# Optimization experiments

Hardware: AMD Instinct MI355X
Metric: run time of the kernel (lower is better)

The kernel has to match this reference:

```python
import jax, jax.numpy as jnp
import numpy as np

B, T, D, H = 4, 2048, 1024, 16
HD = D // H


def setup_inputs() -> dict:
    key = jax.random.key(0)
    ks = jax.random.split(key, 6)
    s = 0.02
    return {
        "x": jax.random.normal(ks[0], (B, T, D), dtype=jnp.float32),
        "padding_mask": jnp.zeros((B, T), dtype=bool),
        "Wq": jax.random.normal(ks[1], (D, D), dtype=jnp.float32) * s,
        "Wk": jax.random.normal(ks[2], (D, D), dtype=jnp.float32) * s,
        "Wv": jax.random.normal(ks[3], (D, D), dtype=jnp.float32) * s,
        "Wo": jax.random.normal(ks[4], (D, D), dtype=jnp.float32) * s,
        "bo": jax.random.normal(ks[5], (D,), dtype=jnp.float32) * s,
    }


def reference(x, padding_mask, Wq, Wk, Wv, Wo, bo):
    # torch nn.Linear: y = x @ W.T
    b, t, d = x.shape
    q = (x @ Wq.T).reshape(b, t, H, HD).transpose(0, 2, 1, 3)  # [B,H,T,hd]
    k = (x @ Wk.T).reshape(b, t, H, HD).transpose(0, 2, 1, 3)
    v = (x @ Wv.T).reshape(b, t, H, HD).transpose(0, 2, 1, 3)

    scores = jnp.einsum("bhid,bhjd->bhij", q, k) / jnp.sqrt(jnp.float32(HD))
    causal = jnp.tril(jnp.ones((t, t), dtype=bool))  # [T,T]
    neg_inf = jnp.float32(-jnp.inf)
    scores = jnp.where(causal[None, None, :, :], scores, neg_inf)
    scores = jnp.where(padding_mask[:, None, None, :], neg_inf, scores)

    attn = jax.nn.softmax(scores, axis=-1)
    out = jnp.einsum("bhij,bhjd->bhid", attn, v)
    out = out.transpose(0, 2, 1, 3).reshape(b, t, d)
    out = out @ Wo.T + bo
    nonpad = (~padding_mask)[:, :, None].astype(out.dtype)
    return out * nonpad
```

## Files before the change

kernel.cpp:

```cpp
#include <hip/hip_runtime.h>

#define B_ 4
#define T_ 2048
#define D_ 1024
#define H_ 16
#define BT_ (B_ * T_)
#define QSCALE (0.125f * 1.44269504088896f)

typedef unsigned short u16;
typedef __attribute__((ext_vector_type(8))) __bf16 bf16x8;
typedef __attribute__((ext_vector_type(4))) float f32x4;

__device__ __forceinline__ u16 f2bf(float f) {
  unsigned u = __builtin_bit_cast(unsigned, f);
  u += 0x7FFFu + ((u >> 16) & 1u);
  return (u16)(u >> 16);
}

__device__ __forceinline__ void gload16(const void* g, void* l) {
  __builtin_amdgcn_global_load_lds(
      (const __attribute__((address_space(1))) void*)g,
      (__attribute__((address_space(3))) void*)l, 16, 0, 0);
}

__global__ void cvt_bf16(const float* __restrict__ in, u16* __restrict__ out, int n4) {
  int i = blockIdx.x * 256 + threadIdx.x;
  if (i >= n4) return;
  const float4 v = ((const float4*)in)[i];
  ushort4 o;
  o.x = f2bf(v.x); o.y = f2bf(v.y); o.z = f2bf(v.z); o.w = f2bf(v.w);
  ((ushort4*)out)[i] = o;
}

__global__ void cvt_wts(const float* __restrict__ Wq, const float* __restrict__ Wk,
                        const float* __restrict__ Wv, const float* __restrict__ Wo,
                        u16* __restrict__ wdst,
                        const unsigned char* __restrict__ pm, unsigned char* __restrict__ fl) {
  const int by = blockIdx.y;
  if (by < 4) {
    const float* src = (by == 0) ? Wq : (by == 1) ? Wk : (by == 2) ? Wv : Wo;
    const int i = blockIdx.x * 256 + threadIdx.x;
    const float4 v = ((const float4*)src)[i];
    ushort4 o;
    o.x = f2bf(v.x); o.y = f2bf(v.y); o.z = f2bf(v.z); o.w = f2bf(v.w);
    ((ushort4*)(wdst + (size_t)by * D_ * D_))[i] = o;
  } else if (blockIdx.x == 0 && threadIdx.x < 128) {
    const int i = threadIdx.x;
    const unsigned long long* p = (const unsigned long long*)(pm + i * 64);
    unsigned long long acc = 0;
#pragma unroll
    for (int k = 0; k < 8; ++k) acc |= p[k];
    fl[i] = acc ? 1 : 0;
  }
}

template<int MODE>
__global__ __launch_bounds__(256, 2) void gemm_bt(
    const u16* __restrict__ A, const u16* __restrict__ Bw,
    float* __restrict__ Cf, const float* __restrict__ bias,
    const unsigned char* __restrict__ rowmask,
    u16* __restrict__ Cq, u16* __restrict__ Ck, u16* __restrict__ Cvt)
{
  __shared__ __align__(16) u16 sA[128 * 64];
  __shared__ __align__(16) u16 sB[128 * 64];
  const int tid = threadIdx.x;
  const int lane = tid & 63, wave = tid >> 6;
  const int g = lane >> 4, s15 = lane & 15;
  const int bm = blockIdx.x * 128, bn = blockIdx.y * 128;
  const int wr = wave >> 1, wc = wave & 1;

  const int srow = lane >> 3;
  const int scol = ((lane & 7) ^ srow) << 3;

  f32x4 acc[4][4] = {};

  for (int kt = 0; kt < 16; ++kt) {
    __syncthreads();
    const int k0 = kt << 6;
#pragma unroll
    for (int c = 0; c < 4; ++c) {
      const int chunk = c * 4 + wave;
      gload16(A  + (size_t)(bm + chunk * 8 + srow) * 1024 + k0 + scol, (char*)sA + chunk * 1024);
      gload16(Bw + (size_t)(bn + chunk * 8 + srow) * 1024 + k0 + scol, (char*)sB + chunk * 1024);
    }
    __syncthreads();
#pragma unroll
    for (int kk = 0; kk < 2; ++kk) {
      const int cb = ((kk << 6) | (g << 4)) ^ ((s15 & 7) << 4);
      bf16x8 af[4], bf[4];
#pragma unroll
      for (int mm = 0; mm < 4; ++mm)
        af[mm] = *(const bf16x8*)((const char*)sA + (wr * 64 + mm * 16 + s15) * 128 + cb);
#pragma unroll
      for (int nn = 0; nn < 4; ++nn)
        bf[nn] = *(const bf16x8*)((const char*)sB + (wc * 64 + nn * 16 + s15) * 128 + cb);
#pragma unroll
      for (int mm = 0; mm < 4; ++mm)
#pragma unroll
        for (int nn = 0; nn < 4; ++nn)
          acc[mm][nn] = __builtin_amdgcn_mfma_f32_16x16x32_bf16(af[mm], bf[nn], acc[mm][nn], 0, 0, 0);
    }
  }

  if (MODE == 1) {
    const int region = bn >> 10;
    const float a = (region == 0) ? QSCALE : 1.f;
#pragma unroll
    for (int mm = 0; mm < 4; ++mm)
#pragma unroll
      for (int nn = 0; nn < 4; ++nn) {
        const int col = bn + wc * 64 + nn * 16 + s15;
        const int colr = col & 1023;
        const int row0 = bm + wr * 64 + mm * 16 + (g << 2);
        if (region == 2) {
          ushort4 w;
          w.x = f2bf(acc[mm][nn][0]); w.y = f2bf(acc[mm][nn][1]);
          w.z = f2bf(acc[mm][nn][2]); w.w = f2bf(acc[mm][nn][3]);
          *(ushort4*)(Cvt + (size_t)colr * BT_ + row0) = w;
        } else {
          u16* dst = region ? Ck : Cq;
#pragma unroll
          for (int r = 0; r < 4; ++r)
            dst[(size_t)(row0 + r) * 1024 + colr] = f2bf(acc[mm][nn][r] * a);
        }
      }
  } else {
#pragma unroll
    for (int mm = 0; mm < 4; ++mm)
#pragma unroll
      for (int nn = 0; nn < 4; ++nn) {
        const int col = bn + wc * 64 + nn * 16 + s15;
        const int row0 = bm + wr * 64 + mm * 16 + (g << 2);
        const float bv = bias[col];
#pragma unroll
        for (int r = 0; r < 4; ++r) {
          float v = acc[mm][nn][r] + bv;
          v = rowmask[row0 + r] ? 0.f : v;
          Cf[(size_t)(row0 + r) * 1024 + col] = v;
        }
      }
  }
}

__global__ __launch_bounds__(512, 4) void attn_fwd(
    const u16* __restrict__ Q, const u16* __restrict__ K,
    const u16* __restrict__ VT, const unsigned char* __restrict__ pm,
    const unsigned char* __restrict__ tileflag, u16* __restrict__ O)
{
  __shared__ __align__(16) u16 sK[2][64 * 64];
  __shared__ __align__(16) u16 sV[2][64 * 64];
  const int tid = threadIdx.x;
  const int lane = tid & 63, wave = tid >> 6;
  const int g = lane >> 4, s15 = lane & 15;
  const int bh = blockIdx.x, b = bh >> 4, h = bh & 15;
  const int qt = blockIdx.y;
  const size_t tokbase = (size_t)b * T_;

  const int srow = tid >> 3;
  const int sc = (tid & 7) ^ (srow & 7);
  const u16* Kb0 = K + tokbase * D_ + h * 64 + sc * 8;
  const u16* Vb0 = VT + (size_t)(h * 64) * BT_ + tokbase + sc * 8;

  const int q0 = qt * 128;
  const int qw = q0 + wave * 16;
  const int nt = 2 * qt + 2;

  bf16x8 qf[2];
#pragma unroll
  for (int ks = 0; ks < 2; ++ks)
    qf[ks] = *(const bf16x8*)(Q + (tokbase + qw + s15) * D_ + h * 64 + ks * 32 + g * 8);

  f32x4 o[4] = {};
  float l_ = 0.f;

  gload16(Kb0 + (size_t)srow * D_,  (char*)(&sK[0][0]) + tid * 16);
  gload16(Vb0 + (size_t)srow * BT_, (char*)(&sV[0][0]) + tid * 16);
  __syncthreads();

  for (int t = 0; t < nt; ++t) {
    const int kv0 = t << 6;
    if (t + 1 < nt) {
      const int nb = (t + 1) & 1;
      gload16(Kb0 + (size_t)(kv0 + 64 + srow) * D_,  (char*)(&sK[nb][0]) + tid * 16);
      gload16(Vb0 + (size_t)srow * BT_ + kv0 + 64,   (char*)(&sV[nb][0]) + tid * 16);
    }

    if (kv0 <= qw + 15) {
      const u16* kb_ = &sK[t & 1][0];
      const u16* vb_ = &sV[t & 1][0];

      f32x4 st[4] = {};
#pragma unroll
      for (int ks = 0; ks < 2; ++ks) {
        bf16x8 kf[4];
#pragma unroll
        for (int jf = 0; jf < 4; ++jf)
          kf[jf] = *(const bf16x8*)(kb_ + (jf * 16 + s15) * 64 + (((ks * 4 + g) ^ (s15 & 7)) << 3));
        __builtin_amdgcn_s_setprio(1);
#pragma unroll
        for (int jf = 0; jf < 4; ++jf)
          st[jf] = __builtin_amdgcn_mfma_f32_16x16x32_bf16(kf[jf], qf[ks], st[jf], 0, 0, 0);
        __builtin_amdgcn_s_setprio(0);
      }

      if (kv0 + 63 > qw) {
        const int iq = qw + s15;
#pragma unroll
        for (int jf = 0; jf < 4; ++jf) {
          const int jb = kv0 + jf * 16 + g * 4;
#pragma unroll
          for (int r = 0; r < 4; ++r)
            if (jb + r > iq) st[jf][r] = -1e30f;
        }
      }
      if (tileflag[b * 32 + t]) {
#pragma unroll
        for (int jf = 0; jf < 4; ++jf) {
          const int jb = kv0 + jf * 16 + g * 4;
          uchar4 p4 = *(const uchar4*)(pm + b * T_ + jb);
          const unsigned char* pr = (const unsigned char*)&p4;
#pragma unroll
          for (int r = 0; r < 4; ++r)
            if (pr[r]) st[jf][r] = -1e30f;
        }
      }

#pragma unroll
      for (int jf = 0; jf < 4; ++jf)
#pragma unroll
        for (int r = 0; r < 4; ++r) {
          const float p = __builtin_amdgcn_exp2f(st[jf][r]);
          st[jf][r] = p;
          l_ += p;
        }

#pragma unroll
      for (int kb2 = 0; kb2 < 2; ++kb2) {
        bf16x8 vf[4];
#pragma unroll
        for (int df = 0; df < 4; ++df)
          vf[df] = *(const bf16x8*)(vb_ + (df * 16 + s15) * 64 + (((kb2 * 4 + g) ^ (s15 & 7)) << 3));
        unsigned w00, w01, w10, w11;
        asm("v_cvt_pk_bf16_f32 %0, %1, %2" : "=v"(w00) : "v"(st[2*kb2][0]),   "v"(st[2*kb2][1]));
        asm("v_cvt_pk_bf16_f32 %0, %1, %2" : "=v"(w01) : "v"(st[2*kb2][2]),   "v"(st[2*kb2][3]));
        asm("v_cvt_pk_bf16_f32 %0, %1, %2" : "=v"(w10) : "v"(st[2*kb2+1][0]), "v"(st[2*kb2+1][1]));
        asm("v_cvt_pk_bf16_f32 %0, %1, %2" : "=v"(w11) : "v"(st[2*kb2+1][2]), "v"(st[2*kb2+1][3]));
        asm("v_permlane32_swap_b32 %0, %1" : "+v"(w00), "+v"(w10));
        asm("v_permlane16_swap_b32 %0, %1" : "+v"(w00), "+v"(w10));
        asm("v_permlane32_swap_b32 %0, %1" : "+v"(w01), "+v"(w11));
        asm("v_permlane16_swap_b32 %0, %1" : "+v"(w01), "+v"(w11));
        union { unsigned u[4]; bf16x8 v; } pf;
        pf.u[0] = w00; pf.u[1] = w01; pf.u[2] = w10; pf.u[3] = w11;
        __builtin_amdgcn_s_setprio(1);
#pragma unroll
        for (int df = 0; df < 4; ++df)
          o[df] = __builtin_amdgcn_mfma_f32_16x16x32_bf16(vf[df], pf.v, o[df], 0, 0, 0);
        __builtin_amdgcn_s_setprio(0);
      }
    }
    __syncthreads();
  }

  l_ += __shfl_xor(l_, 16);
  l_ += __shfl_xor(l_, 32);
  const float inv = 1.f / l_;
  u16* orow = O + (tokbase + qw + s15) * D_ + h * 64 + g * 4;
#pragma unroll
  for (int df = 0; df < 4; ++df) {
    ushort4 w;
    w.x = f2bf(o[df][0] * inv); w.y = f2bf(o[df][1] * inv);
    w.z = f2bf(o[df][2] * inv); w.w = f2bf(o[df][3] * inv);
    *(ushort4*)(orow + df * 16) = w;
  }
}

extern "C" void kernel_launch(void* const* d_in, const int* in_sizes, int n_in,
                              void* d_out, int out_size, void* d_ws, size_t ws_size,
                              hipStream_t stream)
{
  const float* x  = (const float*)d_in[0];
  const unsigned char* pm = (const unsigned char*)d_in[1];
  const float* Wq = (const float*)d_in[2];
  const float* Wk = (const float*)d_in[3];
  const float* Wv = (const float*)d_in[4];
  const float* Wo = (const float*)d_in[5];
  const float* bo = (const float*)d_in[6];
  float* out = (float*)d_out;

  char* w = (char*)d_ws;
  u16* xb  = (u16*)w; w += (size_t)BT_ * D_ * 2;
  u16* wqb = (u16*)w; w += (size_t)D_ * D_ * 2;
  u16* wkb = (u16*)w; w += (size_t)D_ * D_ * 2;
  u16* wvb = (u16*)w; w += (size_t)D_ * D_ * 2;
  u16* wob = (u16*)w; w += (size_t)D_ * D_ * 2;
  u16* qb  = (u16*)w; w += (size_t)BT_ * D_ * 2;
  u16* kbf = (u16*)w; w += (size_t)BT_ * D_ * 2;
  u16* vt  = (u16*)w; w += (size_t)BT_ * D_ * 2;
  u16* ao  = (u16*)w; w += (size_t)BT_ * D_ * 2;
  unsigned char* flags = (unsigned char*)w; w += 256;
  (void)wkb; (void)wvb;

  const int nx4 = BT_ * D_ / 4;
  cvt_bf16<<<nx4 / 256, 256, 0, stream>>>(x, xb, nx4);
  cvt_wts<<<dim3(1024, 5), 256, 0, stream>>>(Wq, Wk, Wv, Wo, wqb, pm, flags);

  gemm_bt<1><<<dim3(64, 24), 256, 0, stream>>>(xb, wqb, nullptr, nullptr, nullptr, qb, kbf, vt);

  attn_fwd<<<dim3(B_ * H_, 16), 512, 0, stream>>>(qb, kbf, vt, pm, flags, ao);

  gemm_bt<0><<<dim3(64, 8), 256, 0, stream>>>(ao, wob, out, bo, pm, nullptr, nullptr, nullptr);
}
```

Baseline: 149.9 us.

## Pair causal query tiles per block and software-pipeline QK with 4-stage KV ring

Each attention block now processes two query tiles (qt and 15-qt) so causal work is balanced across blocks, halving the grid. The KV staging grows from double to quad buffering with loads issued three tiles ahead and explicit vmcnt waits instead of full syncthreads. The QK MFMA for the next tile is computed before the softmax/PV of the current tile to overlap matrix and vector work, and padding tile flags are preloaded into registers. This raises LDS use and register pressure, which may reduce occupancy.

```diff
diff --git a/kernel.cpp b/kernel.cpp
--- a/kernel.cpp
+++ b/kernel.cpp
@@ -8,6 +8,7 @@
 #define QSCALE (0.125f * 1.44269504088896f)
 
 typedef unsigned short u16;
+typedef unsigned long long u64;
 typedef __attribute__((ext_vector_type(8))) __bf16 bf16x8;
 typedef __attribute__((ext_vector_type(4))) float f32x4;
 
@@ -142,18 +143,113 @@
   }
 }
 
+#define QK_TILE(T, ST) do {                                                    \
+  const int kvq_ = (T) << 6;                                                   \
+  _Pragma("unroll")                                                            \
+  for (int jf_ = 0; jf_ < 4; ++jf_) ST[jf_] = f32x4{};                         \
+  if (kvq_ <= qw + 15) {                                                       \
+    const u16* kbq_ = &sK[(T) & 3][0];                                         \
+    _Pragma("unroll")                                                          \
+    for (int ks_ = 0; ks_ < 2; ++ks_) {                                        \
+      bf16x8 kf_[4];                                                           \
+      _Pragma("unroll")                                                        \
+      for (int jf_ = 0; jf_ < 4; ++jf_)                                        \
+        kf_[jf_] = *(const bf16x8*)(kbq_ + (jf_ * 16 + s15) * 64 +             \
+                                    (((ks_ * 4 + g) ^ (s15 & 7)) << 3));       \
+      __builtin_amdgcn_s_setprio(1);                                           \
+      _Pragma("unroll")                                                        \
+      for (int jf_ = 0; jf_ < 4; ++jf_)                                        \
+        ST[jf_] = __builtin_amdgcn_mfma_f32_16x16x32_bf16(kf_[jf_], qf[ks_],   \
+                                                          ST[jf_], 0, 0, 0);   \
+      __builtin_amdgcn_s_setprio(0);                                           \
+    }                                                                          \
+  }                                                                            \
+} while (0)
+
+#define ATTN_ITER(T, CUR, NXT) do {                                            \
+  const int kv0_ = (T) << 6;                                                   \
+  if ((T) + 3 < nt) {                                                          \
+    const int s_ = ((T) + 3) & 3;                                              \
+    gload16(Kb0 + (size_t)(kv0_ + 192 + srow) * D_, (char*)(&sK[s_][0]) + tid * 16); \
+    gload16(Vb0 + (size_t)srow * BT_ + kv0_ + 192,  (char*)(&sV[s_][0]) + tid * 16); \
+  }                                                                            \
+  if ((T) + 1 < nt) QK_TILE((T) + 1, NXT);                                     \
+  if (kv0_ <= qw + 15) {                                                       \
+    if (kv0_ + 63 > qw) {                                                      \
+      const int iq_ = qw + s15;                                                \
+      _Pragma("unroll")                                                        \
+      for (int jf_ = 0; jf_ < 4; ++jf_) {                                      \
+        const int jb_ = kv0_ + jf_ * 16 + g * 4;                               \
+        _Pragma("unroll")                                                      \
+        for (int r_ = 0; r_ < 4; ++r_)                                         \
+          if (jb_ + r_ > iq_) CUR[jf_][r_] = -1e30f;                           \
+      }                                                                        \
+    }                                                                          \
+    if ((flq[(T) >> 3] >> (((T) & 7) * 8)) & 0xff) {                           \
+      _Pragma("unroll")                                                        \
+      for (int jf_ = 0; jf_ < 4; ++jf_) {                                      \
+        const int jb_ = kv0_ + jf_ * 16 + g * 4;                               \
+        uchar4 p4_ = *(const uchar4*)(pm + b * T_ + jb_);                      \
+        const unsigned char* pr_ = (const unsigned char*)&p4_;                 \
+        _Pragma("unroll")                                                      \
+        for (int r_ = 0; r_ < 4; ++r_)                                         \
+          if (pr_[r_]) CUR[jf_][r_] = -1e30f;                                  \
+      }                                                                        \
+    }                                                                          \
+    _Pragma("unroll")                                                          \
+    for (int jf_ = 0; jf_ < 4; ++jf_) {                                        \
+      _Pragma("unroll")                                                        \
+      for (int r_ = 0; r_ < 4; ++r_)                                           \
+        CUR[jf_][r_] = __builtin_amdgcn_exp2f(CUR[jf_][r_]);                   \
+      l4 += CUR[jf_];                                                          \
+    }                                                                          \
+    const u16* vbq_ = &sV[(T) & 3][0];                                         \
+    _Pragma("unroll")                                                          \
+    for (int kb_ = 0; kb_ < 2; ++kb_) {                                        \
+      bf16x8 vf_[4];                                                           \
+      _Pragma("unroll")                                                        \
+      for (int df_ = 0; df_ < 4; ++df_)                                        \
+        vf_[df_] = *(const bf16x8*)(vbq_ + (df_ * 16 + s15) * 64 +             \
+                                    (((kb_ * 4 + g) ^ (s15 & 7)) << 3));       \
+      unsigned w00, w01, w10, w11;                                             \
+      asm("v_cvt_pk_bf16_f32 %0, %1, %2" : "=v"(w00) : "v"(CUR[2*kb_][0]),   "v"(CUR[2*kb_][1]));   \
+      asm("v_cvt_pk_bf16_f32 %0, %1, %2" : "=v"(w01) : "v"(CUR[2*kb_][2]),   "v"(CUR[2*kb_][3]));   \
+      asm("v_cvt_pk_bf16_f32 %0, %1, %2" : "=v"(w10) : "v"(CUR[2*kb_+1][0]), "v"(CUR[2*kb_+1][1])); \
+      asm("v_cvt_pk_bf16_f32 %0, %1, %2" : "=v"(w11) : "v"(CUR[2*kb_+1][2]), "v"(CUR[2*kb_+1][3])); \
+      asm("v_permlane32_swap_b32 %0, %1" : "+v"(w00), "+v"(w10));              \
+      asm("v_permlane16_swap_b32 %0, %1" : "+v"(w00), "+v"(w10));              \
+      asm("v_permlane32_swap_b32 %0, %1" : "+v"(w01), "+v"(w11));              \
+      asm("v_permlane16_swap_b32 %0, %1" : "+v"(w01), "+v"(w11));              \
+      union { unsigned u[4]; bf16x8 v; } pf_;                                  \
+      pf_.u[0] = w00; pf_.u[1] = w01; pf_.u[2] = w10; pf_.u[3] = w11;          \
+      __builtin_amdgcn_s_setprio(1);                                           \
+      _Pragma("unroll")                                                        \
+      for (int df_ = 0; df_ < 4; ++df_)                                        \
+        o[df_] = __builtin_amdgcn_mfma_f32_16x16x32_bf16(vf_[df_], pf_.v,      \
+                                                         o[df_], 0, 0, 0);     \
+      __builtin_amdgcn_s_setprio(0);                                           \
+    }                                                                          \
+  }                                                                            \
+  if ((T) + 1 < nt) {                                                          \
+    if ((T) + 3 < nt) asm volatile("s_waitcnt vmcnt(2) lgkmcnt(0)" ::: "memory"); \
+    else              asm volatile("s_waitcnt vmcnt(0) lgkmcnt(0)" ::: "memory"); \
+    __builtin_amdgcn_s_barrier();                                              \
+    asm volatile("" ::: "memory");                                             \
+  }                                                                            \
+} while (0)
+
 __global__ __launch_bounds__(512, 4) void attn_fwd(
     const u16* __restrict__ Q, const u16* __restrict__ K,
     const u16* __restrict__ VT, const unsigned char* __restrict__ pm,
     const unsigned char* __restrict__ tileflag, u16* __restrict__ O)
 {
-  __shared__ __align__(16) u16 sK[2][64 * 64];
-  __shared__ __align__(16) u16 sV[2][64 * 64];
+  __shared__ __align__(16) u16 sK[4][64 * 64];
+  __shared__ __align__(16) u16 sV[4][64 * 64];
   const int tid = threadIdx.x;
   const int lane = tid & 63, wave = tid >> 6;
   const int g = lane >> 4, s15 = lane & 15;
   const int bh = blockIdx.x, b = bh >> 4, h = bh & 15;
-  const int qt = blockIdx.y;
+  const int jpair = blockIdx.y;
   const size_t tokbase = (size_t)b * T_;
 
   const int srow = tid >> 3;
@@ -161,116 +257,54 @@
   const u16* Kb0 = K + tokbase * D_ + h * 64 + sc * 8;
   const u16* Vb0 = VT + (size_t)(h * 64) * BT_ + tokbase + sc * 8;
 
-  const int q0 = qt * 128;
-  const int qw = q0 + wave * 16;
-  const int nt = 2 * qt + 2;
-
-  bf16x8 qf[2];
-#pragma unroll
-  for (int ks = 0; ks < 2; ++ks)
-    qf[ks] = *(const bf16x8*)(Q + (tokbase + qw + s15) * D_ + h * 64 + ks * 32 + g * 8);
-
-  f32x4 o[4] = {};
-  float l_ = 0.f;
-
-  gload16(Kb0 + (size_t)srow * D_,  (char*)(&sK[0][0]) + tid * 16);
-  gload16(Vb0 + (size_t)srow * BT_, (char*)(&sV[0][0]) + tid * 16);
-  __syncthreads();
-
-  for (int t = 0; t < nt; ++t) {
-    const int kv0 = t << 6;
-    if (t + 1 < nt) {
-      const int nb = (t + 1) & 1;
-      gload16(Kb0 + (size_t)(kv0 + 64 + srow) * D_,  (char*)(&sK[nb][0]) + tid * 16);
-      gload16(Vb0 + (size_t)srow * BT_ + kv0 + 64,   (char*)(&sV[nb][0]) + tid * 16);
-    }
-
-    if (kv0 <= qw + 15) {
-      const u16* kb_ = &sK[t & 1][0];
-      const u16* vb_ = &sV[t & 1][0];
-
-      f32x4 st[4] = {};
-#pragma unroll
-      for (int ks = 0; ks < 2; ++ks) {
-        bf16x8 kf[4];
-#pragma unroll
-        for (int jf = 0; jf < 4; ++jf)
-          kf[jf] = *(const bf16x8*)(kb_ + (jf * 16 + s15) * 64 + (((ks * 4 + g) ^ (s15 & 7)) << 3));
-        __builtin_amdgcn_s_setprio(1);
-#pragma unroll
-        for (int jf = 0; jf < 4; ++jf)
-          st[jf] = __builtin_amdgcn_mfma_f32_16x16x32_bf16(kf[jf], qf[ks], st[jf], 0, 0, 0);
-        __builtin_amdgcn_s_setprio(0);
-      }
-
-      if (kv0 + 63 > qw) {
-        const int iq = qw + s15;
-#pragma unroll
-        for (int jf = 0; jf < 4; ++jf) {
-          const int jb = kv0 + jf * 16 + g * 4;
-#pragma unroll
-          for (int r = 0; r < 4; ++r)
-            if (jb + r > iq) st[jf][r] = -1e30f;
-        }
-      }
-      if (tileflag[b * 32 + t]) {
-#pragma unroll
-        for (int jf = 0; jf < 4; ++jf) {
-          const int jb = kv0 + jf * 16 + g * 4;
-          uchar4 p4 = *(const uchar4*)(pm + b * T_ + jb);
-          const unsigned char* pr = (const unsigned char*)&p4;
-#pragma unroll
-          for (int r = 0; r < 4; ++r)
-            if (pr[r]) st[jf][r] = -1e30f;
-        }
-      }
-
-#pragma unroll
-      for (int jf = 0; jf < 4; ++jf)
-#pragma unroll
-        for (int r = 0; r < 4; ++r) {
-          const float p = __builtin_amdgcn_exp2f(st[jf][r]);
-          st[jf][r] = p;
-          l_ += p;
-        }
-
-#pragma unroll
-      for (int kb2 = 0; kb2 < 2; ++kb2) {
-        bf16x8 vf[4];
-#pragma unroll
-        for (int df = 0; df < 4; ++df)
-          vf[df] = *(const bf16x8*)(vb_ + (df * 16 + s15) * 64 + (((kb2 * 4 + g) ^ (s15 & 7)) << 3));
-        unsigned w00, w01, w10, w11;
-        asm("v_cvt_pk_bf16_f32 %0, %1, %2" : "=v"(w00) : "v"(st[2*kb2][0]),   "v"(st[2*kb2][1]));
-        asm("v_cvt_pk_bf16_f32 %0, %1, %2" : "=v"(w01) : "v"(st[2*kb2][2]),   "v"(st[2*kb2][3]));
-        asm("v_cvt_pk_bf16_f32 %0, %1, %2" : "=v"(w10) : "v"(st[2*kb2+1][0]), "v"(st[2*kb2+1][1]));
-        asm("v_cvt_pk_bf16_f32 %0, %1, %2" : "=v"(w11) : "v"(st[2*kb2+1][2]), "v"(st[2*kb2+1][3]));
-        asm("v_permlane32_swap_b32 %0, %1" : "+v"(w00), "+v"(w10));
-        asm("v_permlane16_swap_b32 %0, %1" : "+v"(w00), "+v"(w10));
-        asm("v_permlane32_swap_b32 %0, %1" : "+v"(w01), "+v"(w11));
-        asm("v_permlane16_swap_b32 %0, %1" : "+v"(w01), "+v"(w11));
-        union { unsigned u[4]; bf16x8 v; } pf;
-        pf.u[0] = w00; pf.u[1] = w01; pf.u[2] = w10; pf.u[3] = w11;
-        __builtin_amdgcn_s_setprio(1);
-#pragma unroll
-        for (int df = 0; df < 4; ++df)
-          o[df] = __builtin_amdgcn_mfma_f32_16x16x32_bf16(vf[df], pf.v, o[df], 0, 0, 0);
-        __builtin_amdgcn_s_setprio(0);
-      }
-    }
+  u64 flq[4];
+#pragma unroll
+  for (int q = 0; q < 4; ++q) flq[q] = ((const u64*)(tileflag + b * 32))[q];
+
+#pragma unroll
+  for (int half = 0; half < 2; ++half) {
+    const int qt = half ? (15 - jpair) : jpair;
+    const int qw = qt * 128 + wave * 16;
+    const int nt = 2 * qt + 2;
+
+    bf16x8 qf[2];
+#pragma unroll
+    for (int ks = 0; ks < 2; ++ks)
+      qf[ks] = *(const bf16x8*)(Q + (tokbase + qw + s15) * D_ + h * 64 + ks * 32 + g * 8);
+
+    f32x4 o[4] = {};
+    f32x4 l4 = {};
+
     __syncthreads();
-  }
-
-  l_ += __shfl_xor(l_, 16);
-  l_ += __shfl_xor(l_, 32);
-  const float inv = 1.f / l_;
-  u16* orow = O + (tokbase + qw + s15) * D_ + h * 64 + g * 4;
-#pragma unroll
-  for (int df = 0; df < 4; ++df) {
-    ushort4 w;
-    w.x = f2bf(o[df][0] * inv); w.y = f2bf(o[df][1] * inv);
-    w.z = f2bf(o[df][2] * inv); w.w = f2bf(o[df][3] * inv);
-    *(ushort4*)(orow + df * 16) = w;
+#pragma unroll
+    for (int s = 0; s < 3; ++s) {
+      gload16(Kb0 + (size_t)(s * 64 + srow) * D_, (char*)(&sK[s][0]) + tid * 16);
+      gload16(Vb0 + (size_t)srow * BT_ + s * 64,  (char*)(&sV[s][0]) + tid * 16);
+    }
+    asm volatile("s_waitcnt vmcnt(2) lgkmcnt(0)" ::: "memory");
+    __builtin_amdgcn_s_barrier();
+    asm volatile("" ::: "memory");
+
+    f32x4 stA[4], stB[4];
+    QK_TILE(0, stA);
+
+    for (int t = 0; t < nt; t += 2) {
+      ATTN_ITER(t, stA, stB);
+      ATTN_ITER(t + 1, stB, stA);
+    }
+
+    float lv = (l4[0] + l4[1]) + (l4[2] + l4[3]);
+    lv += __shfl_xor(lv, 16);
+    lv += __shfl_xor(lv, 32);
+    const float inv = 1.f / lv;
+    u16* orow = O + (tokbase + qw + s15) * D_ + h * 64 + g * 4;
+#pragma unroll
+    for (int df = 0; df < 4; ++df) {
+      ushort4 w;
+      w.x = f2bf(o[df][0] * inv); w.y = f2bf(o[df][1] * inv);
+      w.z = f2bf(o[df][2] * inv); w.w = f2bf(o[df][3] * inv);
+      *(ushort4*)(orow + df * 16) = w;
+    }
   }
 }
 
@@ -306,7 +340,7 @@
 
   gemm_bt<1><<<dim3(64, 24), 256, 0, stream>>>(xb, wqb, nullptr, nullptr, nullptr, qb, kbf, vt);
 
-  attn_fwd<<<dim3(B_ * H_, 16), 512, 0, stream>>>(qb, kbf, vt, pm, flags, ao);
+  attn_fwd<<<dim3(B_ * H_, 8), 512, 0, stream>>>(qb, kbf, vt, pm, flags, ao);
 
   gemm_bt<0><<<dim3(64, 8), 256, 0, stream>>>(ao, wob, out, bo, pm, nullptr, nullptr, nullptr);
 }
```

New measurement: 142.8 us. 1.05x faster.
